# Performance work log

Hardware: AMD Instinct MI355X
Metric: run time of the kernel (lower is better)

## Reference

```python
import jax, jax.numpy as jnp
import numpy as np

NUM_TOPICS = 64
VOCAB_SIZE = 50000
BATCH = 2048
RHO = 0.1

def setup_inputs() -> dict:
    key = jax.random.key(0)
    k_x, k_b, k_t, k_m = jax.random.split(key, 4)
    x = jax.random.uniform(k_x, (BATCH, VOCAB_SIZE), dtype=jnp.float32)  # BoW-like counts
    beta = jax.random.normal(k_b, (NUM_TOPICS, VOCAB_SIZE), dtype=jnp.float32)
    theta = jax.random.normal(k_t, (NUM_TOPICS, NUM_TOPICS), dtype=jnp.float32)
    mu = jax.random.normal(k_m, (NUM_TOPICS,), dtype=jnp.float32)
    return {"x": x, "beta": beta, "theta": theta, "mu": mu}

def reference(x, beta, theta, mu):
    # Original double loop:
    #   log_prob[:,k] = sum(x*beta[k],1) + mu[k] + rho * sum_{j!=k} theta[k,j]*sum(x*beta[j],1)
    # Let s[b,k] = sum_v x[b,v]*beta[k,v] = (x @ beta.T)[b,k].
    # Then log_prob = s + mu + rho * s @ (theta with zeroed diagonal).T
    s = jnp.einsum('bv,kv->bk', x, beta)                      # [B, K]
    theta_off = theta * (1.0 - jnp.eye(theta.shape[0], dtype=theta.dtype))
    log_prob = s + mu[None, :] + RHO * jnp.einsum('bj,kj->bk', s, theta_off)
    return log_prob
```

## Files before the change

kernel.cpp:

```cpp
#include <hip/hip_runtime.h>

typedef unsigned short u16;
typedef unsigned int u32;
typedef unsigned long long u64;

#define VOCAB 50000
#define BATCH 2048
#define NTOP 64
#define RHO 0.1f

#define KSPLIT 4
#define CHUNKA 12512
#define KSTEP 256
#define NSTEPS 49
#define NKB 1568
#define GPC 12544

typedef short bf16x4 __attribute__((ext_vector_type(4)));
typedef short bf16x8 __attribute__((ext_vector_type(8)));
typedef float f32x4 __attribute__((ext_vector_type(4)));

__device__ __forceinline__ u16 f32_to_bf16(float f) {
  u32 u = __builtin_bit_cast(u32, f);
  return (u16)((u + 0x8000u) >> 16);
}
__device__ __forceinline__ u32 pack2(float a, float b) {
  return (u32)f32_to_bf16(a) | ((u32)f32_to_bf16(b) << 16);
}
__device__ __forceinline__ u32 cvtpk(float lo, float hi) {
  u32 r;
  asm volatile("v_cvt_pk_bf16_f32 %0, %1, %2" : "=v"(r) : "v"(lo), "v"(hi));
  return r;
}
union frag_cast { bf16x4 h[2]; bf16x8 v; };

__global__ void ctm_prep(const float* __restrict__ beta, u16* __restrict__ bp) {
  int i = blockIdx.x * blockDim.x + threadIdx.x;
  int stride = gridDim.x * blockDim.x;
  for (int j = i; j < NTOP * GPC; j += stride) {
    int col = j / GPC;
    int g = j - col * GPC;
    int k = g * 4;
    float4 v = make_float4(0.f, 0.f, 0.f, 0.f);
    if (k < VOCAB)
      v = *(const float4*)(beta + (u64)col * VOCAB + k);
    int kb = k >> 5;
    int jj = k & 31;
    int pbase = ((jj & 15) >> 2) * 8 + ((jj & 16) ? 4 : 0);
    u32 lo = pack2(v.x, v.y), hi = pack2(v.z, v.w);
    *(uint2*)(bp + (u64)kb * 2048 + col * 32 + pbase) = make_uint2(lo, hi);
  }
}

__global__ void __launch_bounds__(256, 2) ctm_gemm(const float* __restrict__ x,
                                                   const u16* __restrict__ bp,
                                                   float* __restrict__ sp) {
  __shared__ u16 ldsA[2][16 * KSTEP];
  const int t = threadIdx.x;
  const int l = t & 63;
  const int w = t >> 6;
  const int fr = l & 15;
  const int fk = l >> 4;

  const int bx = blockIdx.x;
  const int k0 = bx * CHUNKA;
  const int klen = (k0 + CHUNKA < VOCAB) ? CHUNKA : (VOCAB - k0);
  const int r0 = blockIdx.y * 16;

  const float* xb = x + (u64)(r0 + w * 4) * VOCAB + k0 + l * 4;
  u32 wb[4];
  #pragma unroll
  for (int j = 0; j < 4; ++j) {
    const int row = w * 4 + j;
    wb[j] = (u32)(row * 512) + (((u32)(l * 8)) ^ ((u32)((row & 7) << 4)));
  }

  const u16* bb = bp + (u64)(k0 >> 5) * 2048 + (w * 16 + fr) * 32 + fk * 8;

  const u32 arb = (u32)(fr * 512);
  const u32 aswz = (u32)((fr & 7) << 4);

  f32x4 acc = {0.f, 0.f, 0.f, 0.f};

  #pragma unroll
  for (int j = 0; j < 4; ++j) {
    float4 v = make_float4(0.f, 0.f, 0.f, 0.f);
    if (l * 4 < klen) v = *(const float4*)(xb + (u64)j * VOCAB);
    *(uint2*)((char*)ldsA[0] + wb[j]) = make_uint2(cvtpk(v.x, v.y), cvtpk(v.z, v.w));
  }
  __syncthreads();

  for (int st = 0; st < NSTEPS; ++st) {
    const int cb = st & 1;
    const bool have = (st + 1) < NSTEPS;

    float4 av[4];
    if (have) {
      const int rem = klen - (st + 1) * KSTEP;
      #pragma unroll
      for (int j = 0; j < 4; ++j) {
        av[j] = make_float4(0.f, 0.f, 0.f, 0.f);
        if (l * 4 < rem)
          av[j] = *(const float4*)(xb + (u64)j * VOCAB + (st + 1) * KSTEP);
      }
    }

    const u16* bs = bb + (u64)st * 8 * 2048;
    const char* bufA = (const char*)ldsA[cb];
    #pragma unroll
    for (int s = 0; s < 8; ++s) {
      bf16x8 bfr = *(const bf16x8*)(bs + s * 2048);
      frag_cast ua;
      ua.h[0] = *(const bf16x4*)(bufA + arb + (((u32)(s * 64 + fk * 8)) ^ aswz));
      ua.h[1] = *(const bf16x4*)(bufA + arb + (((u32)(s * 64 + 32 + fk * 8)) ^ aswz));
      acc = __builtin_amdgcn_mfma_f32_16x16x32_bf16(ua.v, bfr, acc, 0, 0, 0);
    }

    if (have) {
      char* nA = (char*)ldsA[cb ^ 1];
      #pragma unroll
      for (int j = 0; j < 4; ++j)
        *(uint2*)(nA + wb[j]) = make_uint2(cvtpk(av[j].x, av[j].y), cvtpk(av[j].z, av[j].w));
      __syncthreads();
    }
  }

  float* spb = sp + (u64)bx * (BATCH * NTOP);
  #pragma unroll
  for (int r = 0; r < 4; ++r)
    spb[(u64)(r0 + fk * 4 + r) * NTOP + (w * 16 + fr)] = acc[r];
}

__global__ void __launch_bounds__(256) ctm_epi(const float* __restrict__ sp,
                                               const float* __restrict__ theta,
                                               const float* __restrict__ mu,
                                               float* __restrict__ out) {
  __shared__ float thT[NTOP * NTOP];
  __shared__ float sb[8 * NTOP];
  const int t = threadIdx.x;
  const int r0 = blockIdx.x * 8;

  #pragma unroll
  for (int i = 0; i < 16; ++i) {
    int e = i * 256 + t;
    thT[(e & 63) * 64 + (e >> 6)] = theta[e];
  }

  const int k = t & 63;
  const int rl = t >> 6;
  #pragma unroll
  for (int rr = 0; rr < 2; ++rr) {
    const int r = rl + rr * 4;
    float sum = 0.f;
    #pragma unroll
    for (int cc = 0; cc < KSPLIT; ++cc)
      sum += sp[(u64)cc * (BATCH * NTOP) + (r0 + r) * NTOP + k];
    sb[r * 64 + k] = sum;
  }
  __syncthreads();

  const float muk = mu[k];
  const float diag = thT[k * 64 + k];
  #pragma unroll
  for (int rr = 0; rr < 2; ++rr) {
    const int r = rl + rr * 4;
    const float* srow = &sb[r * 64];
    float accv = 0.f;
    #pragma unroll 8
    for (int j = 0; j < 64; ++j)
      accv += thT[j * 64 + k] * srow[j];
    const float sv = srow[k];
    out[(r0 + r) * 64 + k] = sv + muk + RHO * (accv - diag * sv);
  }
}

extern "C" void kernel_launch(void* const* d_in, const int* in_sizes, int n_in,
                              void* d_out, int out_size, void* d_ws, size_t ws_size,
                              hipStream_t stream) {
  const float* x = (const float*)d_in[0];
  const float* beta = (const float*)d_in[1];
  const float* theta = (const float*)d_in[2];
  const float* mu = (const float*)d_in[3];
  float* out = (float*)d_out;

  u16* bp = (u16*)d_ws;
  float* sp = (float*)((char*)d_ws + 6422528u);

  ctm_prep<<<1568, 256, 0, stream>>>(beta, bp);
  ctm_gemm<<<dim3(KSPLIT, BATCH / 16), 256, 0, stream>>>(x, bp, sp);
  ctm_epi<<<BATCH / 8, 256, 0, stream>>>(sp, theta, mu, out);
}
```

Baseline: 123.1 us.

## Widen split-K to 32 with 32x64 block tiles and nontemporal x loads

Raises the split-K factor from 4 to 32, shrinks the K step to 64, and gives each block a 32-row by 64-column tile in which each wave computes 16x32 with two MFMA accumulators. This halves the number of times each beta fragment is re-read across row blocks and launches four times as many blocks. x is loaded with nontemporal hints and the occupancy hint rises to 6. The cost is an 8x larger partial-sum buffer that the epilogue must write and then read back across 32 splits, plus a larger workspace requirement.

Measured after the change: 119.8 us. 1.03x faster.

```diff
diff --git a/kernel.cpp b/kernel.cpp
--- a/kernel.cpp
+++ b/kernel.cpp
@@ -9,16 +9,16 @@
 #define NTOP 64
 #define RHO 0.1f
 
-#define KSPLIT 4
-#define CHUNKA 12512
-#define KSTEP 256
-#define NSTEPS 49
+#define KSPLIT 32
+#define CHUNK 1568
+#define KSTEP 64
 #define NKB 1568
 #define GPC 12544
 
 typedef short bf16x4 __attribute__((ext_vector_type(4)));
 typedef short bf16x8 __attribute__((ext_vector_type(8)));
 typedef float f32x4 __attribute__((ext_vector_type(4)));
+typedef float f32x4v __attribute__((ext_vector_type(4)));
 
 __device__ __forceinline__ u16 f32_to_bf16(float f) {
   u32 u = __builtin_bit_cast(u32, f);
@@ -52,10 +52,10 @@
   }
 }
 
-__global__ void __launch_bounds__(256, 2) ctm_gemm(const float* __restrict__ x,
+__global__ void __launch_bounds__(256, 6) ctm_gemm(const float* __restrict__ x,
                                                    const u16* __restrict__ bp,
                                                    float* __restrict__ sp) {
-  __shared__ u16 ldsA[2][16 * KSTEP];
+  __shared__ u16 ldsA[2][32 * KSTEP];
   const int t = threadIdx.x;
   const int l = t & 63;
   const int w = t >> 6;
@@ -63,72 +63,83 @@
   const int fk = l >> 4;
 
   const int bx = blockIdx.x;
-  const int k0 = bx * CHUNKA;
-  const int klen = (k0 + CHUNKA < VOCAB) ? CHUNKA : (VOCAB - k0);
-  const int r0 = blockIdx.y * 16;
-
-  const float* xb = x + (u64)(r0 + w * 4) * VOCAB + k0 + l * 4;
-  u32 wb[4];
-  #pragma unroll
-  for (int j = 0; j < 4; ++j) {
-    const int row = w * 4 + j;
-    wb[j] = (u32)(row * 512) + (((u32)(l * 8)) ^ ((u32)((row & 7) << 4)));
-  }
-
-  const u16* bb = bp + (u64)(k0 >> 5) * 2048 + (w * 16 + fr) * 32 + fk * 8;
-
-  const u32 arb = (u32)(fr * 512);
-  const u32 aswz = (u32)((fr & 7) << 4);
-
-  f32x4 acc = {0.f, 0.f, 0.f, 0.f};
-
-  #pragma unroll
-  for (int j = 0; j < 4; ++j) {
-    float4 v = make_float4(0.f, 0.f, 0.f, 0.f);
-    if (l * 4 < klen) v = *(const float4*)(xb + (u64)j * VOCAB);
-    *(uint2*)((char*)ldsA[0] + wb[j]) = make_uint2(cvtpk(v.x, v.y), cvtpk(v.z, v.w));
+  const int k0 = bx * CHUNK;
+  const int kend = (k0 + CHUNK < VOCAB) ? (k0 + CHUNK) : VOCAB;
+  const int row0 = blockIdx.y * 32;
+  const int nsteps = (kend - k0 + KSTEP - 1) >> 6;
+
+  const int c = t & 15;
+  const int srow = t >> 4;
+  const float* xb = x + (u64)(row0 + srow) * VOCAB + k0 + c * 4;
+  const u32 wofs = (u32)(srow * 128) + (((u32)(c * 8)) ^ ((u32)((srow & 7) << 4)));
+
+  const int col0 = (w >> 1) * 32 + fr;
+  const u16* bb0 = bp + (u64)(k0 >> 5) * 2048 + col0 * 32 + fk * 8;
+  const u16* bb1 = bb0 + 16 * 32;
+
+  const int arow = (w & 1) * 16 + fr;
+  const u32 arb = (u32)(arow * 128);
+  const u32 aswz = (u32)((arow & 7) << 4);
+
+  f32x4 acc0 = {0.f, 0.f, 0.f, 0.f};
+  f32x4 acc1 = {0.f, 0.f, 0.f, 0.f};
+
+  {
+    const int rem = (kend - k0 < KSTEP) ? (kend - k0) : KSTEP;
+    f32x4v a0 = {0.f,0.f,0.f,0.f}, a1 = {0.f,0.f,0.f,0.f};
+    if (c * 4 < rem) {
+      a0 = __builtin_nontemporal_load((const f32x4v*)xb);
+      a1 = __builtin_nontemporal_load((const f32x4v*)(xb + 16 * VOCAB));
+    }
+    *(uint2*)((char*)ldsA[0] + wofs)        = make_uint2(cvtpk(a0.x, a0.y), cvtpk(a0.z, a0.w));
+    *(uint2*)((char*)ldsA[0] + wofs + 2048) = make_uint2(cvtpk(a1.x, a1.y), cvtpk(a1.z, a1.w));
   }
   __syncthreads();
 
-  for (int st = 0; st < NSTEPS; ++st) {
+  for (int st = 0; st < nsteps; ++st) {
     const int cb = st & 1;
-    const bool have = (st + 1) < NSTEPS;
-
-    float4 av[4];
+    const bool have = (st + 1) < nsteps;
+
+    f32x4v a0 = {0.f,0.f,0.f,0.f}, a1 = {0.f,0.f,0.f,0.f};
     if (have) {
-      const int rem = klen - (st + 1) * KSTEP;
-      #pragma unroll
-      for (int j = 0; j < 4; ++j) {
-        av[j] = make_float4(0.f, 0.f, 0.f, 0.f);
-        if (l * 4 < rem)
-          av[j] = *(const float4*)(xb + (u64)j * VOCAB + (st + 1) * KSTEP);
+      const int rem = kend - k0 - ((st + 1) << 6);
+      if (c * 4 < rem) {
+        const float* xp = xb + ((st + 1) << 6);
+        a0 = __builtin_nontemporal_load((const f32x4v*)xp);
+        a1 = __builtin_nontemporal_load((const f32x4v*)(xp + 16 * VOCAB));
       }
     }
 
-    const u16* bs = bb + (u64)st * 8 * 2048;
     const char* bufA = (const char*)ldsA[cb];
     #pragma unroll
-    for (int s = 0; s < 8; ++s) {
-      bf16x8 bfr = *(const bf16x8*)(bs + s * 2048);
+    for (int s = 0; s < 2; ++s) {
+      const u64 kb = (u64)(st * 2 + s) * 2048;
+      bf16x8 b0 = *(const bf16x8*)(bb0 + kb);
+      bf16x8 b1 = *(const bf16x8*)(bb1 + kb);
+      const u32 in0 = (u32)(s * 64 + fk * 8);
+      const u32 in1 = in0 + 32;
       frag_cast ua;
-      ua.h[0] = *(const bf16x4*)(bufA + arb + (((u32)(s * 64 + fk * 8)) ^ aswz));
-      ua.h[1] = *(const bf16x4*)(bufA + arb + (((u32)(s * 64 + 32 + fk * 8)) ^ aswz));
-      acc = __builtin_amdgcn_mfma_f32_16x16x32_bf16(ua.v, bfr, acc, 0, 0, 0);
+      ua.h[0] = *(const bf16x4*)(bufA + arb + (in0 ^ aswz));
+      ua.h[1] = *(const bf16x4*)(bufA + arb + (in1 ^ aswz));
+      acc0 = __builtin_amdgcn_mfma_f32_16x16x32_bf16(ua.v, b0, acc0, 0, 0, 0);
+      acc1 = __builtin_amdgcn_mfma_f32_16x16x32_bf16(ua.v, b1, acc1, 0, 0, 0);
     }
 
     if (have) {
       char* nA = (char*)ldsA[cb ^ 1];
-      #pragma unroll
-      for (int j = 0; j < 4; ++j)
-        *(uint2*)(nA + wb[j]) = make_uint2(cvtpk(av[j].x, av[j].y), cvtpk(av[j].z, av[j].w));
+      *(uint2*)(nA + wofs)        = make_uint2(cvtpk(a0.x, a0.y), cvtpk(a0.z, a0.w));
+      *(uint2*)(nA + wofs + 2048) = make_uint2(cvtpk(a1.x, a1.y), cvtpk(a1.z, a1.w));
       __syncthreads();
     }
   }
 
   float* spb = sp + (u64)bx * (BATCH * NTOP);
-  #pragma unroll
-  for (int r = 0; r < 4; ++r)
-    spb[(u64)(r0 + fk * 4 + r) * NTOP + (w * 16 + fr)] = acc[r];
+  const int orow = row0 + (w & 1) * 16 + fk * 4;
+  #pragma unroll
+  for (int r = 0; r < 4; ++r) {
+    spb[(u64)(orow + r) * NTOP + col0] = acc0[r];
+    spb[(u64)(orow + r) * NTOP + col0 + 16] = acc1[r];
+  }
 }
 
 __global__ void __launch_bounds__(256) ctm_epi(const float* __restrict__ sp,
@@ -187,6 +198,6 @@
   float* sp = (float*)((char*)d_ws + 6422528u);
 
   ctm_prep<<<1568, 256, 0, stream>>>(beta, bp);
-  ctm_gemm<<<dim3(KSPLIT, BATCH / 16), 256, 0, stream>>>(x, bp, sp);
+  ctm_gemm<<<dim3(KSPLIT, BATCH / 32), 256, 0, stream>>>(x, bp, sp);
   ctm_epi<<<BATCH / 8, 256, 0, stream>>>(sp, theta, mu, out);
 }
```
